# Kernel optimization log

Hardware: AMD Instinct MI355X
Metric: run time of the kernel (lower is better)

The kernel has to match this reference:

```python
import jax, jax.numpy as jnp
import numpy as np

B, T, D, H = 4, 2048, 1024, 16
Dh = D // H          # 64 head dim
NF = Dh // 2         # 32 rotary frequencies


def setup_inputs() -> dict:
    key = jax.random.key(0)
    k0, k1, k2, k3 = jax.random.split(key, 4)
    x = jax.random.normal(k0, (B, T, D), dtype=jnp.float32)
    # 3D spatial coordinates per token, e.g. voxel positions
    coords = jax.random.uniform(k1, (B, T, 3), dtype=jnp.float32, minval=0.0, maxval=64.0)
    w_scale = 1.0 / np.sqrt(D)
    qkv_w = jax.random.normal(k2, (3 * D, D), dtype=jnp.float32) * w_scale
    qkv_b = jnp.zeros((3 * D,), dtype=jnp.float32)
    proj_w = jax.random.normal(k3, (D, D), dtype=jnp.float32) * w_scale
    proj_b = jnp.zeros((D,), dtype=jnp.float32)
    # mixed-axis rope: frequency f uses coordinate axis (f % 3), geometric period spacing within each axis group
    axes = (jnp.arange(NF) % 3).astype(jnp.int32)
    group = (jnp.arange(NF) // 3).astype(jnp.float32)
    n_per_axis = float(NF) / 3.0
    inv_freq = (10000.0 ** (-group / n_per_axis)).astype(jnp.float32)
    return {"x": x, "coords": coords, "qkv_w": qkv_w, "qkv_b": qkv_b,
            "proj_w": proj_w, "proj_b": proj_b, "inv_freq": inv_freq, "axes": axes}


def _apply_rope(t, sin, cos):
    # t: [B, H, T, Dh]; sin/cos: [B, 1, T, Dh//2]  (rotate-half convention)
    t1, t2 = jnp.split(t, 2, axis=-1)
    return jnp.concatenate([t1 * cos - t2 * sin, t1 * sin + t2 * cos], axis=-1)


def reference(x, coords, qkv_w, qkv_b, proj_w, proj_b, inv_freq, axes):
    b, t, d = x.shape
    # fused QKV projection
    qkv = (x @ qkv_w.T + qkv_b).reshape(b, t, 3, H, Dh)
    qkv = jnp.transpose(qkv, (2, 0, 3, 1, 4))     # [3, B, H, T, Dh]
    q, k, v = qkv[0], qkv[1], qkv[2]
    # vectorized per-sample rope from coords (replaces python loop over batch)
    ang = jnp.take(coords, axes, axis=-1) * inv_freq      # [B, T, NF]
    sin = jnp.sin(ang)[:, None]                            # [B, 1, T, NF]
    cos = jnp.cos(ang)[:, None]
    q = _apply_rope(q, sin, cos)
    k = _apply_rope(k, sin, cos)
    # standard scaling mode: single 1/sqrt(Dh) inside SDPA
    scale = 1.0 / np.sqrt(Dh)
    scores = jnp.einsum('bhqd,bhkd->bhqk', q, k) * scale
    attn = jax.nn.softmax(scores, axis=-1)
    out = jnp.einsum('bhqk,bhkd->bhqd', attn, v)           # [B, H, T, Dh]
    out = jnp.transpose(out, (0, 2, 1, 3)).reshape(b, t, d)
    return out @ proj_w.T + proj_b
```

## Files before the change

### kernel.cpp

```cpp
#include <hip/hip_runtime.h>
#include <hip/hip_bf16.h>

#define B_ 4
#define T_ 2048
#define D_ 1024
#define H_ 16
#define DH 64
#define NF 32
#define BH (B_*H_)
#define M_ROWS (B_*T_)

#define QSCALE 0.125f

using u16 = unsigned short;
using u32 = unsigned int;

typedef __bf16 bf16x8 __attribute__((ext_vector_type(8)));
typedef float  f32x4  __attribute__((ext_vector_type(4)));
typedef float  f32x16 __attribute__((ext_vector_type(16)));

__device__ __forceinline__ u16 f2bf(float f) {
  u32 u = __float_as_uint(f);
  u32 r = u + 0x7fffu + ((u >> 16) & 1u);
  return (u16)(r >> 16);
}
__device__ __forceinline__ u16 f2bf_hw(float f) {
  __bf16 h = (__bf16)f;
  return *(u16*)&h;
}
__device__ __forceinline__ u32 pack2(float lo, float hi) {
  return (u32)f2bf_hw(lo) | ((u32)f2bf_hw(hi) << 16);
}
__device__ __forceinline__ float bf2f(u16 h) {
  return __uint_as_float(((u32)h) << 16);
}

__device__ __forceinline__ void pl32swap(u32 a, u32 b, u32& x, u32& y) {
  x = a; y = b;
  asm("s_nop 1\n\t"
      "v_permlane32_swap_b32 %0, %1"
      : "+v"(x), "+v"(y));
}

__device__ __forceinline__ void gload_lds16(const void* g, void* l) {
  __builtin_amdgcn_global_load_lds((__attribute__((address_space(1))) void*)(g),
                                   (__attribute__((address_space(3))) void*)(l),
                                   16, 0, 0);
}

__global__ __launch_bounds__(256)
void cvt_kernel(const float* __restrict__ in, u16* __restrict__ out, int n8) {
  int idx = blockIdx.x * 256 + threadIdx.x;
  if (idx >= n8) return;
  const float4* p = (const float4*)in + (long)idx * 2;
  float4 a = p[0], b = p[1];
  u32 o0 = (u32)f2bf(a.x) | ((u32)f2bf(a.y) << 16);
  u32 o1 = (u32)f2bf(a.z) | ((u32)f2bf(a.w) << 16);
  u32 o2 = (u32)f2bf(b.x) | ((u32)f2bf(b.y) << 16);
  u32 o3 = (u32)f2bf(b.z) | ((u32)f2bf(b.w) << 16);
  ((uint4*)out)[idx] = make_uint4(o0, o1, o2, o3);
}

__global__ __launch_bounds__(256)
void sincos_kernel(const float* __restrict__ coords, const float* __restrict__ inv_freq,
                   const int* __restrict__ axes, float* __restrict__ sc) {
  int idx = blockIdx.x * 256 + threadIdx.x;
  if (idx >= B_ * T_ * NF) return;
  int f = idx & 31;
  long bt = idx >> 5;
  float c = coords[bt * 3 + axes[f]];
  float ang = c * inv_freq[f];
  sc[bt * 64 + f]      = sinf(ang);
  sc[bt * 64 + 32 + f] = cosf(ang);
}

__global__ __launch_bounds__(256, 2)
void gemm_qkv(const u16* __restrict__ A, const u16* __restrict__ Bt,
              const float* __restrict__ bias, const float* __restrict__ sc,
              u16* __restrict__ qr, u16* __restrict__ kr, u16* __restrict__ vbuf) {
  const int N = 3 * D_, K = D_;
  __shared__ u16 As[128 * 64];
  __shared__ u16 Bs[128 * 64];
  int nb = N >> 7;
  int bid = blockIdx.x;
  int nwg = gridDim.x;
  int cpx = nwg >> 3;
  bid = (bid & 7) * cpx + (bid >> 3);
  int bm = bid / nb, bn = bid % nb;
  long m0 = (long)bm << 7, n0 = (long)bn << 7;
  int tid = threadIdx.x;
  int lane = tid & 63, w = tid >> 6;
  int g = lane >> 4, lr = lane & 15;
  int wm = w >> 1, wn = w & 1;

  f32x4 acc[4][4] = {};

  for (int kt = 0; kt < K; kt += 64) {
    __syncthreads();
    #pragma unroll
    for (int j = 0; j < 4; ++j) {
      int ob = j * 4096 + tid * 16;
      int row = ob >> 7, col = (ob & 127) >> 1;
      u16* ldsA = As + j * 2048 + w * 512;
      u16* ldsB = Bs + j * 2048 + w * 512;
      gload_lds16(A + (m0 + row) * K + kt + col, ldsA);
      gload_lds16(Bt + (n0 + row) * K + kt + col, ldsB);
    }
    __syncthreads();
    #pragma unroll
    for (int kk = 0; kk < 2; ++kk) {
      bf16x8 af[4], bfr[4];
      #pragma unroll
      for (int i = 0; i < 4; ++i)
        af[i] = *(const bf16x8*)(As + (wm * 64 + i * 16 + lr) * 64 + kk * 32 + g * 8);
      #pragma unroll
      for (int i = 0; i < 4; ++i)
        bfr[i] = *(const bf16x8*)(Bs + (wn * 64 + i * 16 + lr) * 64 + kk * 32 + g * 8);
      #pragma unroll
      for (int mi = 0; mi < 4; ++mi)
        #pragma unroll
        for (int nj = 0; nj < 4; ++nj)
          acc[mi][nj] = __builtin_amdgcn_mfma_f32_16x16x32_bf16(af[mi], bfr[nj], acc[mi][nj], 0, 0, 0);
    }
  }

  int part = (int)(n0 >> 10);
  int h = ((int)(n0 & 1023) >> 6) + wn;
  float bv[4];
  #pragma unroll
  for (int nj = 0; nj < 4; ++nj)
    bv[nj] = bias[n0 + wn * 64 + nj * 16 + lr];

  #pragma unroll
  for (int mi = 0; mi < 4; ++mi) {
    #pragma unroll
    for (int i = 0; i < 4; ++i) {
      long row = m0 + wm * 64 + mi * 16 + g * 4 + i;
      int b = (int)(row >> 11), t = (int)(row & 2047);
      long obase = ((long)(b * 16 + h) * T_ + t) * 64;
      if (part == 2) {
        #pragma unroll
        for (int nj = 0; nj < 4; ++nj)
          vbuf[obase + nj * 16 + lr] = f2bf(acc[mi][nj][i] + bv[nj]);
      } else {
        u16* outp = part ? kr : qr;
        float fac = part ? 1.0f : QSCALE;
        const float* scp = sc + row * 64;
        #pragma unroll
        for (int nj = 0; nj < 2; ++nj) {
          int d = nj * 16 + lr;
          float sn = scp[d], cs = scp[32 + d];
          float t1 = acc[mi][nj][i]     + bv[nj];
          float t2 = acc[mi][nj + 2][i] + bv[nj + 2];
          outp[obase + d]      = f2bf((t1 * cs - t2 * sn) * fac);
          outp[obase + 32 + d] = f2bf((t1 * sn + t2 * cs) * fac);
        }
      }
    }
  }
}

__global__ __launch_bounds__(256, 2)
void gemm_bt(const u16* __restrict__ A, const u16* __restrict__ Bt,
             const float* __restrict__ bias, float* __restrict__ Cout,
             int M, int N, int K) {
  __shared__ u16 As[128 * 64];
  __shared__ u16 Bs[128 * 64];
  int nb = N >> 7;
  int bid = blockIdx.x;
  int nwg = gridDim.x;
  if ((nwg & 7) == 0) {
    int c = nwg >> 3;
    bid = (bid & 7) * c + (bid >> 3);
  }
  int bm = bid / nb, bn = bid % nb;
  long m0 = (long)bm << 7, n0 = (long)bn << 7;
  int tid = threadIdx.x;
  int lane = tid & 63, w = tid >> 6;
  int g = lane >> 4, lr = lane & 15;
  int wm = w >> 1, wn = w & 1;

  f32x4 acc[4][4] = {};

  for (int kt = 0; kt < K; kt += 64) {
    __syncthreads();
    #pragma unroll
    for (int j = 0; j < 4; ++j) {
      int ob = j * 4096 + tid * 16;
      int row = ob >> 7, col = (ob & 127) >> 1;
      u16* ldsA = As + j * 2048 + w * 512;
      u16* ldsB = Bs + j * 2048 + w * 512;
      gload_lds16(A + (m0 + row) * K + kt + col, ldsA);
      gload_lds16(Bt + (n0 + row) * K + kt + col, ldsB);
    }
    __syncthreads();
    #pragma unroll
    for (int kk = 0; kk < 2; ++kk) {
      bf16x8 af[4], bfr[4];
      #pragma unroll
      for (int i = 0; i < 4; ++i)
        af[i] = *(const bf16x8*)(As + (wm * 64 + i * 16 + lr) * 64 + kk * 32 + g * 8);
      #pragma unroll
      for (int i = 0; i < 4; ++i)
        bfr[i] = *(const bf16x8*)(Bs + (wn * 64 + i * 16 + lr) * 64 + kk * 32 + g * 8);
      #pragma unroll
      for (int mi = 0; mi < 4; ++mi)
        #pragma unroll
        for (int nj = 0; nj < 4; ++nj)
          acc[mi][nj] = __builtin_amdgcn_mfma_f32_16x16x32_bf16(af[mi], bfr[nj], acc[mi][nj], 0, 0, 0);
    }
  }
  #pragma unroll
  for (int mi = 0; mi < 4; ++mi) {
    #pragma unroll
    for (int nj = 0; nj < 4; ++nj) {
      long col = n0 + wn * 64 + nj * 16 + lr;
      float bvv = bias[col];
      #pragma unroll
      for (int i = 0; i < 4; ++i) {
        long row = m0 + wm * 64 + mi * 16 + g * 4 + i;
        Cout[row * (long)N + col] = acc[mi][nj][i] + bvv;
      }
    }
  }
}

__global__ __launch_bounds__(256)
void vtrans_kernel(const u16* __restrict__ vbuf, u16* __restrict__ vt) {
  __shared__ u16 Vsm[128 * 72];
  int bh = blockIdx.y;
  int t0 = blockIdx.x << 7;
  int tid = threadIdx.x;
  #pragma unroll
  for (int it = 0; it < 4; ++it) {
    int item = it * 256 + tid;
    int tl = item >> 3, dg = item & 7;
    uint4 u = *(const uint4*)(vbuf + ((long)bh * T_ + t0 + tl) * 64 + dg * 8);
    *(uint4*)(Vsm + tl * 72 + dg * 8) = u;
  }
  __syncthreads();
  int d = tid >> 2, tc = tid & 3;
  long obase = ((long)bh * DH + d) * T_ + t0 + tc * 32;
  #pragma unroll
  for (int c = 0; c < 4; ++c) {
    u32 o[4];
    #pragma unroll
    for (int j = 0; j < 4; ++j) {
      u16 lo = Vsm[(tc * 32 + c * 8 + 2 * j)     * 72 + d];
      u16 hi = Vsm[(tc * 32 + c * 8 + 2 * j + 1) * 72 + d];
      o[j] = (u32)lo | ((u32)hi << 16);
    }
    *(uint4*)(vt + obase + c * 8) = make_uint4(o[0], o[1], o[2], o[3]);
  }
}

__global__ __launch_bounds__(256, 2)
void attn_kernel(const u16* __restrict__ Qr, const u16* __restrict__ Kr,
                 const u16* __restrict__ Vt, u16* __restrict__ Aout) {
  __shared__ u16 Ks[2][64 * 64];
  __shared__ u16 Vs[2][64 * 64];
  int wg = (blockIdx.x & 7) * 64 + (blockIdx.x >> 3);
  int bh = wg >> 3;
  int b = bh >> 4, h = bh & 15;
  int q0 = (wg & 7) << 8;
  int tid = threadIdx.x;
  int lane = tid & 63, w = tid >> 6;
  int l5 = lane & 31, hb = lane >> 5;

  const long tbase = (long)bh * T_;
  const long vbase = (long)bh * DH;
  const int qs = q0 + w * 64;

  bf16x8 bq0[4], bq1[4];
  #pragma unroll
  for (int s = 0; s < 4; ++s) {
    bq0[s] = *(const bf16x8*)(Qr + (tbase + qs + l5)      * DH + s * 16 + hb * 8);
    bq1[s] = *(const bf16x8*)(Qr + (tbase + qs + 32 + l5) * DH + s * 16 + hb * 8);
  }

  f32x16 oa00 = {}, oa01 = {};
  f32x16 oa10 = {}, oa11 = {};
  float ls0 = 0.f, ls1 = 0.f;

  const int sl = l5 & 7;

  auto STAGE = [&](int buf, int kb) {
    #pragma unroll
    for (int j = 0; j < 2; ++j) {
      int ob = j * 4096 + tid * 16;
      int row = ob >> 7;
      int c = ((ob >> 4) & 7) ^ (row & 7);
      u16* ldsK = Ks[buf] + j * 2048 + w * 512;
      u16* ldsV = Vs[buf] + j * 2048 + w * 512;
      gload_lds16(Kr + (tbase + kb + row) * DH + c * 8, ldsK);
      gload_lds16(Vt + (vbase + row) * T_ + kb + c * 8, ldsV);
    }
  };

  STAGE(0, 0);
  asm volatile("s_waitcnt vmcnt(0)" ::: "memory");
  __builtin_amdgcn_s_barrier();
  __builtin_amdgcn_sched_barrier(0);

  int cur = 0;
  for (int kt = 0; kt < T_ / 64; ++kt) {
    if (kt + 1 < T_ / 64) STAGE(cur ^ 1, (kt + 1) * 64);

    const u16* kbuf = Ks[cur];
    const u16* vbuf = Vs[cur];

    f32x16 p00 = {}, p01 = {}, p10 = {}, p11 = {};
    #pragma unroll
    for (int s = 0; s < 4; ++s) {
      int c = ((2 * s + hb) ^ sl) * 8;
      bf16x8 ak0 = *(const bf16x8*)(kbuf + l5 * 64 + c);
      bf16x8 ak1 = *(const bf16x8*)(kbuf + (32 + l5) * 64 + c);
      p00 = __builtin_amdgcn_mfma_f32_32x32x16_bf16(ak0, bq0[s], p00, 0, 0, 0);
      p01 = __builtin_amdgcn_mfma_f32_32x32x16_bf16(ak1, bq0[s], p01, 0, 0, 0);
      p10 = __builtin_amdgcn_mfma_f32_32x32x16_bf16(ak0, bq1[s], p10, 0, 0, 0);
      p11 = __builtin_amdgcn_mfma_f32_32x32x16_bf16(ak1, bq1[s], p11, 0, 0, 0);
    }

    u32 pA0[8], pB0[8], pA1[8], pB1[8];
    #pragma unroll
    for (int r4 = 0; r4 < 4; ++r4) {
      float a0 = __expf(p00[4 * r4 + 0]), a1 = __expf(p00[4 * r4 + 1]);
      float a2 = __expf(p00[4 * r4 + 2]), a3 = __expf(p00[4 * r4 + 3]);
      ls0 += (a0 + a1) + (a2 + a3);
      pA0[r4] = pack2(a0, a1); pB0[r4] = pack2(a2, a3);
      float b0 = __expf(p01[4 * r4 + 0]), b1 = __expf(p01[4 * r4 + 1]);
      float b2 = __expf(p01[4 * r4 + 2]), b3 = __expf(p01[4 * r4 + 3]);
      ls0 += (b0 + b1) + (b2 + b3);
      pA0[4 + r4] = pack2(b0, b1); pB0[4 + r4] = pack2(b2, b3);
      float c0 = __expf(p10[4 * r4 + 0]), c1 = __expf(p10[4 * r4 + 1]);
      float c2 = __expf(p10[4 * r4 + 2]), c3 = __expf(p10[4 * r4 + 3]);
      ls1 += (c0 + c1) + (c2 + c3);
      pA1[r4] = pack2(c0, c1); pB1[r4] = pack2(c2, c3);
      float d0 = __expf(p11[4 * r4 + 0]), d1 = __expf(p11[4 * r4 + 1]);
      float d2 = __expf(p11[4 * r4 + 2]), d3 = __expf(p11[4 * r4 + 3]);
      ls1 += (d0 + d1) + (d2 + d3);
      pA1[4 + r4] = pack2(d0, d1); pB1[4 + r4] = pack2(d2, d3);
    }

    #pragma unroll
    for (int s2 = 0; s2 < 4; ++s2) {
      int c = ((2 * s2 + hb) ^ sl) * 8;
      bf16x8 av0 = *(const bf16x8*)(vbuf + l5 * 64 + c);
      bf16x8 av1 = *(const bf16x8*)(vbuf + (32 + l5) * 64 + c);
      u32 w0, w1, w2, w3;
      pl32swap(pA0[2 * s2], pA0[2 * s2 + 1], w0, w2);
      pl32swap(pB0[2 * s2], pB0[2 * s2 + 1], w1, w3);
      union { u32 u[4]; bf16x8 v; } bw0;
      bw0.u[0] = w0; bw0.u[1] = w1; bw0.u[2] = w2; bw0.u[3] = w3;
      oa00 = __builtin_amdgcn_mfma_f32_32x32x16_bf16(av0, bw0.v, oa00, 0, 0, 0);
      oa01 = __builtin_amdgcn_mfma_f32_32x32x16_bf16(av1, bw0.v, oa01, 0, 0, 0);
      pl32swap(pA1[2 * s2], pA1[2 * s2 + 1], w0, w2);
      pl32swap(pB1[2 * s2], pB1[2 * s2 + 1], w1, w3);
      union { u32 u[4]; bf16x8 v; } bw1;
      bw1.u[0] = w0; bw1.u[1] = w1; bw1.u[2] = w2; bw1.u[3] = w3;
      oa10 = __builtin_amdgcn_mfma_f32_32x32x16_bf16(av0, bw1.v, oa10, 0, 0, 0);
      oa11 = __builtin_amdgcn_mfma_f32_32x32x16_bf16(av1, bw1.v, oa11, 0, 0, 0);
    }

    __builtin_amdgcn_sched_barrier(0);
    asm volatile("s_waitcnt vmcnt(0)" ::: "memory");
    __builtin_amdgcn_s_barrier();
    __builtin_amdgcn_sched_barrier(0);
    cur ^= 1;
  }

  ls0 += __shfl_xor(ls0, 32);
  ls1 += __shfl_xor(ls1, 32);
  float inv0 = 1.0f / ls0;
  float inv1 = 1.0f / ls1;
  long row0 = (long)b * T_ + qs + l5;
  u16* ob0 = Aout + row0 * D_ + h * DH;
  u16* ob1 = ob0 + 32 * D_;
  #pragma unroll
  for (int r4 = 0; r4 < 4; ++r4) {
    u32 w0 = pack2(oa00[4 * r4 + 0] * inv0, oa00[4 * r4 + 1] * inv0);
    u32 w1 = pack2(oa00[4 * r4 + 2] * inv0, oa00[4 * r4 + 3] * inv0);
    *(uint2*)(ob0 + r4 * 8 + hb * 4) = make_uint2(w0, w1);
    u32 w2 = pack2(oa01[4 * r4 + 0] * inv0, oa01[4 * r4 + 1] * inv0);
    u32 w3 = pack2(oa01[4 * r4 + 2] * inv0, oa01[4 * r4 + 3] * inv0);
    *(uint2*)(ob0 + 32 + r4 * 8 + hb * 4) = make_uint2(w2, w3);
    u32 w4 = pack2(oa10[4 * r4 + 0] * inv1, oa10[4 * r4 + 1] * inv1);
    u32 w5 = pack2(oa10[4 * r4 + 2] * inv1, oa10[4 * r4 + 3] * inv1);
    *(uint2*)(ob1 + r4 * 8 + hb * 4) = make_uint2(w4, w5);
    u32 w6 = pack2(oa11[4 * r4 + 0] * inv1, oa11[4 * r4 + 1] * inv1);
    u32 w7 = pack2(oa11[4 * r4 + 2] * inv1, oa11[4 * r4 + 3] * inv1);
    *(uint2*)(ob1 + 32 + r4 * 8 + hb * 4) = make_uint2(w6, w7);
  }
}

extern "C" void kernel_launch(void* const* d_in, const int* in_sizes, int n_in,
                              void* d_out, int out_size, void* d_ws, size_t ws_size,
                              hipStream_t stream) {
  const float* x        = (const float*)d_in[0];
  const float* coords   = (const float*)d_in[1];
  const float* qkv_w    = (const float*)d_in[2];
  const float* qkv_b    = (const float*)d_in[3];
  const float* proj_w   = (const float*)d_in[4];
  const float* proj_b   = (const float*)d_in[5];
  const float* inv_freq = (const float*)d_in[6];
  const int*   axes     = (const int*)d_in[7];
  float* out = (float*)d_out;

  char* ws = (char*)d_ws;
  size_t off = 0;
  auto alloc = [&](size_t bytes) -> char* {
    char* p = ws + off;
    off += (bytes + 255) & ~(size_t)255;
    return p;
  };
  u16*   xb     = (u16*)  alloc((size_t)M_ROWS * D_ * 2);
  u16*   wqkv   = (u16*)  alloc((size_t)3 * D_ * D_ * 2);
  u16*   wproj  = (u16*)  alloc((size_t)D_ * D_ * 2);
  float* sc     = (float*)alloc((size_t)M_ROWS * 64 * 4);
  u16*   qr     = (u16*)  alloc((size_t)BH * T_ * DH * 2);
  u16*   kr     = (u16*)  alloc((size_t)BH * T_ * DH * 2);
  u16*   vbuf   = (u16*)  alloc((size_t)BH * T_ * DH * 2);
  u16*   vt     = (u16*)  alloc((size_t)BH * T_ * DH * 2);
  u16*   aout   = vbuf;

  cvt_kernel<<<(M_ROWS * D_ / 8 + 255) / 256, 256, 0, stream>>>(x, xb, M_ROWS * D_ / 8);
  cvt_kernel<<<(3 * D_ * D_ / 8 + 255) / 256, 256, 0, stream>>>(qkv_w, wqkv, 3 * D_ * D_ / 8);
  cvt_kernel<<<(D_ * D_ / 8 + 255) / 256, 256, 0, stream>>>(proj_w, wproj, D_ * D_ / 8);
  sincos_kernel<<<(B_ * T_ * NF + 255) / 256, 256, 0, stream>>>(coords, inv_freq, axes, sc);

  gemm_qkv<<<(M_ROWS / 128) * (3 * D_ / 128), 256, 0, stream>>>(xb, wqkv, qkv_b, sc,
                                                                qr, kr, vbuf);
  vtrans_kernel<<<dim3(T_ / 128, BH), 256, 0, stream>>>(vbuf, vt);
  attn_kernel<<<512, 256, 0, stream>>>(qr, kr, vt, aout);
  gemm_bt<<<(M_ROWS / 128) * (D_ / 128), 256, 0, stream>>>(aout, wproj, proj_b, out,
                                                           M_ROWS, D_, D_);
}
```

Baseline: 214.4 us.

## Fuse V transpose into QKV GEMM epilogue and stage 128-key blocks in attention

The QKV GEMM epilogue now stages each V head tile in the reused shared memory and writes it out already transposed. This removes the separate vtrans kernel and the round trip of V through an intermediate buffer. Separately, the attention kernel loads K/V in 128-key chunks (two 64-key sub-tiles per stage), halving the number of barrier/wait iterations at the cost of doubling LDS use per workgroup. The larger LDS footprint (64 KB) may limit occupancy, and the GEMM epilogue gains extra syncs for V tiles.

```diff
diff --git a/kernel.cpp b/kernel.cpp
--- a/kernel.cpp
+++ b/kernel.cpp
@@ -77,10 +77,11 @@
 __global__ __launch_bounds__(256, 2)
 void gemm_qkv(const u16* __restrict__ A, const u16* __restrict__ Bt,
               const float* __restrict__ bias, const float* __restrict__ sc,
-              u16* __restrict__ qr, u16* __restrict__ kr, u16* __restrict__ vbuf) {
+              u16* __restrict__ qr, u16* __restrict__ kr, u16* __restrict__ vt) {
   const int N = 3 * D_, K = D_;
-  __shared__ u16 As[128 * 64];
-  __shared__ u16 Bs[128 * 64];
+  __shared__ u16 SMEM[128 * 64 * 2];
+  u16* As = SMEM;
+  u16* Bs = SMEM + 128 * 64;
   int nb = N >> 7;
   int bid = blockIdx.x;
   int nwg = gridDim.x;
@@ -125,26 +126,54 @@
   }
 
   int part = (int)(n0 >> 10);
-  int h = ((int)(n0 & 1023) >> 6) + wn;
+  int b = (int)(m0 >> 11), t0 = (int)(m0 & 2047);
   float bv[4];
   #pragma unroll
   for (int nj = 0; nj < 4; ++nj)
     bv[nj] = bias[n0 + wn * 64 + nj * 16 + lr];
 
-  #pragma unroll
-  for (int mi = 0; mi < 4; ++mi) {
-    #pragma unroll
-    for (int i = 0; i < 4; ++i) {
-      long row = m0 + wm * 64 + mi * 16 + g * 4 + i;
-      int b = (int)(row >> 11), t = (int)(row & 2047);
-      long obase = ((long)(b * 16 + h) * T_ + t) * 64;
-      if (part == 2) {
+  if (part == 2) {
+    int h0 = (int)((n0 & 1023) >> 6);
+    u16* Vsm = SMEM;
+    #pragma unroll
+    for (int hsel = 0; hsel < 2; ++hsel) {
+      __syncthreads();
+      if (wn == hsel) {
         #pragma unroll
-        for (int nj = 0; nj < 4; ++nj)
-          vbuf[obase + nj * 16 + lr] = f2bf(acc[mi][nj][i] + bv[nj]);
-      } else {
-        u16* outp = part ? kr : qr;
-        float fac = part ? 1.0f : QSCALE;
+        for (int mi = 0; mi < 4; ++mi)
+          #pragma unroll
+          for (int i = 0; i < 4; ++i) {
+            int lrow = wm * 64 + mi * 16 + g * 4 + i;
+            #pragma unroll
+            for (int nj = 0; nj < 4; ++nj)
+              Vsm[lrow * 72 + nj * 16 + lr] = f2bf(acc[mi][nj][i] + bv[nj]);
+          }
+      }
+      __syncthreads();
+      int d = tid >> 2, tc = tid & 3;
+      long obase = ((long)((b * 16 + h0 + hsel) * DH + d)) * T_ + t0 + tc * 32;
+      #pragma unroll
+      for (int c = 0; c < 4; ++c) {
+        u32 o[4];
+        #pragma unroll
+        for (int j = 0; j < 4; ++j) {
+          u16 lo = Vsm[(tc * 32 + c * 8 + 2 * j)     * 72 + d];
+          u16 hi = Vsm[(tc * 32 + c * 8 + 2 * j + 1) * 72 + d];
+          o[j] = (u32)lo | ((u32)hi << 16);
+        }
+        *(uint4*)(vt + obase + c * 8) = make_uint4(o[0], o[1], o[2], o[3]);
+      }
+    }
+  } else {
+    int h = ((int)(n0 & 1023) >> 6) + wn;
+    u16* outp = part ? kr : qr;
+    float fac = part ? 1.0f : QSCALE;
+    #pragma unroll
+    for (int mi = 0; mi < 4; ++mi) {
+      #pragma unroll
+      for (int i = 0; i < 4; ++i) {
+        long row = m0 + wm * 64 + mi * 16 + g * 4 + i;
+        long obase = ((long)((b * 16 + h)) * T_ + (row & 2047)) * 64;
         const float* scp = sc + row * 64;
         #pragma unroll
         for (int nj = 0; nj < 2; ++nj) {
@@ -225,40 +254,11 @@
   }
 }
 
-__global__ __launch_bounds__(256)
-void vtrans_kernel(const u16* __restrict__ vbuf, u16* __restrict__ vt) {
-  __shared__ u16 Vsm[128 * 72];
-  int bh = blockIdx.y;
-  int t0 = blockIdx.x << 7;
-  int tid = threadIdx.x;
-  #pragma unroll
-  for (int it = 0; it < 4; ++it) {
-    int item = it * 256 + tid;
-    int tl = item >> 3, dg = item & 7;
-    uint4 u = *(const uint4*)(vbuf + ((long)bh * T_ + t0 + tl) * 64 + dg * 8);
-    *(uint4*)(Vsm + tl * 72 + dg * 8) = u;
-  }
-  __syncthreads();
-  int d = tid >> 2, tc = tid & 3;
-  long obase = ((long)bh * DH + d) * T_ + t0 + tc * 32;
-  #pragma unroll
-  for (int c = 0; c < 4; ++c) {
-    u32 o[4];
-    #pragma unroll
-    for (int j = 0; j < 4; ++j) {
-      u16 lo = Vsm[(tc * 32 + c * 8 + 2 * j)     * 72 + d];
-      u16 hi = Vsm[(tc * 32 + c * 8 + 2 * j + 1) * 72 + d];
-      o[j] = (u32)lo | ((u32)hi << 16);
-    }
-    *(uint4*)(vt + obase + c * 8) = make_uint4(o[0], o[1], o[2], o[3]);
-  }
-}
-
 __global__ __launch_bounds__(256, 2)
 void attn_kernel(const u16* __restrict__ Qr, const u16* __restrict__ Kr,
                  const u16* __restrict__ Vt, u16* __restrict__ Aout) {
-  __shared__ u16 Ks[2][64 * 64];
-  __shared__ u16 Vs[2][64 * 64];
+  __shared__ u16 Ks[2][2][64 * 64];
+  __shared__ u16 Vs[2][2][64 * 64];
   int wg = (blockIdx.x & 7) * 64 + (blockIdx.x >> 3);
   int bh = wg >> 3;
   int b = bh >> 4, h = bh & 15;
@@ -286,14 +286,17 @@
 
   auto STAGE = [&](int buf, int kb) {
     #pragma unroll
-    for (int j = 0; j < 2; ++j) {
-      int ob = j * 4096 + tid * 16;
-      int row = ob >> 7;
-      int c = ((ob >> 4) & 7) ^ (row & 7);
-      u16* ldsK = Ks[buf] + j * 2048 + w * 512;
-      u16* ldsV = Vs[buf] + j * 2048 + w * 512;
-      gload_lds16(Kr + (tbase + kb + row) * DH + c * 8, ldsK);
-      gload_lds16(Vt + (vbase + row) * T_ + kb + c * 8, ldsV);
+    for (int sub = 0; sub < 2; ++sub) {
+      #pragma unroll
+      for (int j = 0; j < 2; ++j) {
+        int ob = j * 4096 + tid * 16;
+        int row = ob >> 7;
+        int c = ((ob >> 4) & 7) ^ (row & 7);
+        u16* ldsK = Ks[buf][sub] + j * 2048 + w * 512;
+        u16* ldsV = Vs[buf][sub] + j * 2048 + w * 512;
+        gload_lds16(Kr + (tbase + kb + sub * 64 + row) * DH + c * 8, ldsK);
+        gload_lds16(Vt + (vbase + row) * T_ + kb + sub * 64 + c * 8, ldsV);
+      }
     }
   };
 
@@ -303,63 +306,66 @@
   __builtin_amdgcn_sched_barrier(0);
 
   int cur = 0;
-  for (int kt = 0; kt < T_ / 64; ++kt) {
-    if (kt + 1 < T_ / 64) STAGE(cur ^ 1, (kt + 1) * 64);
-
-    const u16* kbuf = Ks[cur];
-    const u16* vbuf = Vs[cur];
-
-    f32x16 p00 = {}, p01 = {}, p10 = {}, p11 = {};
-    #pragma unroll
-    for (int s = 0; s < 4; ++s) {
-      int c = ((2 * s + hb) ^ sl) * 8;
-      bf16x8 ak0 = *(const bf16x8*)(kbuf + l5 * 64 + c);
-      bf16x8 ak1 = *(const bf16x8*)(kbuf + (32 + l5) * 64 + c);
-      p00 = __builtin_amdgcn_mfma_f32_32x32x16_bf16(ak0, bq0[s], p00, 0, 0, 0);
-      p01 = __builtin_amdgcn_mfma_f32_32x32x16_bf16(ak1, bq0[s], p01, 0, 0, 0);
-      p10 = __builtin_amdgcn_mfma_f32_32x32x16_bf16(ak0, bq1[s], p10, 0, 0, 0);
-      p11 = __builtin_amdgcn_mfma_f32_32x32x16_bf16(ak1, bq1[s], p11, 0, 0, 0);
-    }
-
-    u32 pA0[8], pB0[8], pA1[8], pB1[8];
-    #pragma unroll
-    for (int r4 = 0; r4 < 4; ++r4) {
-      float a0 = __expf(p00[4 * r4 + 0]), a1 = __expf(p00[4 * r4 + 1]);
-      float a2 = __expf(p00[4 * r4 + 2]), a3 = __expf(p00[4 * r4 + 3]);
-      ls0 += (a0 + a1) + (a2 + a3);
-      pA0[r4] = pack2(a0, a1); pB0[r4] = pack2(a2, a3);
-      float b0 = __expf(p01[4 * r4 + 0]), b1 = __expf(p01[4 * r4 + 1]);
-      float b2 = __expf(p01[4 * r4 + 2]), b3 = __expf(p01[4 * r4 + 3]);
-      ls0 += (b0 + b1) + (b2 + b3);
-      pA0[4 + r4] = pack2(b0, b1); pB0[4 + r4] = pack2(b2, b3);
-      float c0 = __expf(p10[4 * r4 + 0]), c1 = __expf(p10[4 * r4 + 1]);
-      float c2 = __expf(p10[4 * r4 + 2]), c3 = __expf(p10[4 * r4 + 3]);
-      ls1 += (c0 + c1) + (c2 + c3);
-      pA1[r4] = pack2(c0, c1); pB1[r4] = pack2(c2, c3);
-      float d0 = __expf(p11[4 * r4 + 0]), d1 = __expf(p11[4 * r4 + 1]);
-      float d2 = __expf(p11[4 * r4 + 2]), d3 = __expf(p11[4 * r4 + 3]);
-      ls1 += (d0 + d1) + (d2 + d3);
-      pA1[4 + r4] = pack2(d0, d1); pB1[4 + r4] = pack2(d2, d3);
-    }
-
-    #pragma unroll
-    for (int s2 = 0; s2 < 4; ++s2) {
-      int c = ((2 * s2 + hb) ^ sl) * 8;
-      bf16x8 av0 = *(const bf16x8*)(vbuf + l5 * 64 + c);
-      bf16x8 av1 = *(const bf16x8*)(vbuf + (32 + l5) * 64 + c);
-      u32 w0, w1, w2, w3;
-      pl32swap(pA0[2 * s2], pA0[2 * s2 + 1], w0, w2);
-      pl32swap(pB0[2 * s2], pB0[2 * s2 + 1], w1, w3);
-      union { u32 u[4]; bf16x8 v; } bw0;
-      bw0.u[0] = w0; bw0.u[1] = w1; bw0.u[2] = w2; bw0.u[3] = w3;
-      oa00 = __builtin_amdgcn_mfma_f32_32x32x16_bf16(av0, bw0.v, oa00, 0, 0, 0);
-      oa01 = __builtin_amdgcn_mfma_f32_32x32x16_bf16(av1, bw0.v, oa01, 0, 0, 0);
-      pl32swap(pA1[2 * s2], pA1[2 * s2 + 1], w0, w2);
-      pl32swap(pB1[2 * s2], pB1[2 * s2 + 1], w1, w3);
-      union { u32 u[4]; bf16x8 v; } bw1;
-      bw1.u[0] = w0; bw1.u[1] = w1; bw1.u[2] = w2; bw1.u[3] = w3;
-      oa10 = __builtin_amdgcn_mfma_f32_32x32x16_bf16(av0, bw1.v, oa10, 0, 0, 0);
-      oa11 = __builtin_amdgcn_mfma_f32_32x32x16_bf16(av1, bw1.v, oa11, 0, 0, 0);
+  for (int kt = 0; kt < T_ / 128; ++kt) {
+    if (kt + 1 < T_ / 128) STAGE(cur ^ 1, (kt + 1) * 128);
+
+    #pragma unroll
+    for (int h2 = 0; h2 < 2; ++h2) {
+      const u16* kbuf = Ks[cur][h2];
+      const u16* vbuf = Vs[cur][h2];
+
+      f32x16 p00 = {}, p01 = {}, p10 = {}, p11 = {};
+      #pragma unroll
+      for (int s = 0; s < 4; ++s) {
+        int c = ((2 * s + hb) ^ sl) * 8;
+        bf16x8 ak0 = *(const bf16x8*)(kbuf + l5 * 64 + c);
+        bf16x8 ak1 = *(const bf16x8*)(kbuf + (32 + l5) * 64 + c);
+        p00 = __builtin_amdgcn_mfma_f32_32x32x16_bf16(ak0, bq0[s], p00, 0, 0, 0);
+        p01 = __builtin_amdgcn_mfma_f32_32x32x16_bf16(ak1, bq0[s], p01, 0, 0, 0);
+        p10 = __builtin_amdgcn_mfma_f32_32x32x16_bf16(ak0, bq1[s], p10, 0, 0, 0);
+        p11 = __builtin_amdgcn_mfma_f32_32x32x16_bf16(ak1, bq1[s], p11, 0, 0, 0);
+      }
+
+      u32 pA0[8], pB0[8], pA1[8], pB1[8];
+      #pragma unroll
+      for (int r4 = 0; r4 < 4; ++r4) {
+        float a0 = __expf(p00[4 * r4 + 0]), a1 = __expf(p00[4 * r4 + 1]);
+        float a2 = __expf(p00[4 * r4 + 2]), a3 = __expf(p00[4 * r4 + 3]);
+        ls0 += (a0 + a1) + (a2 + a3);
+        pA0[r4] = pack2(a0, a1); pB0[r4] = pack2(a2, a3);
+        float b0 = __expf(p01[4 * r4 + 0]), b1 = __expf(p01[4 * r4 + 1]);
+        float b2 = __expf(p01[4 * r4 + 2]), b3 = __expf(p01[4 * r4 + 3]);
+        ls0 += (b0 + b1) + (b2 + b3);
+        pA0[4 + r4] = pack2(b0, b1); pB0[4 + r4] = pack2(b2, b3);
+        float c0 = __expf(p10[4 * r4 + 0]), c1 = __expf(p10[4 * r4 + 1]);
+        float c2 = __expf(p10[4 * r4 + 2]), c3 = __expf(p10[4 * r4 + 3]);
+        ls1 += (c0 + c1) + (c2 + c3);
+        pA1[r4] = pack2(c0, c1); pB1[r4] = pack2(c2, c3);
+        float d0 = __expf(p11[4 * r4 + 0]), d1 = __expf(p11[4 * r4 + 1]);
+        float d2 = __expf(p11[4 * r4 + 2]), d3 = __expf(p11[4 * r4 + 3]);
+        ls1 += (d0 + d1) + (d2 + d3);
+        pA1[4 + r4] = pack2(d0, d1); pB1[4 + r4] = pack2(d2, d3);
+      }
+
+      #pragma unroll
+      for (int s2 = 0; s2 < 4; ++s2) {
+        int c = ((2 * s2 + hb) ^ sl) * 8;
+        bf16x8 av0 = *(const bf16x8*)(vbuf + l5 * 64 + c);
+        bf16x8 av1 = *(const bf16x8*)(vbuf + (32 + l5) * 64 + c);
+        u32 w0, w1, w2, w3;
+        pl32swap(pA0[2 * s2], pA0[2 * s2 + 1], w0, w2);
+        pl32swap(pB0[2 * s2], pB0[2 * s2 + 1], w1, w3);
+        union { u32 u[4]; bf16x8 v; } bw0;
+        bw0.u[0] = w0; bw0.u[1] = w1; bw0.u[2] = w2; bw0.u[3] = w3;
+        oa00 = __builtin_amdgcn_mfma_f32_32x32x16_bf16(av0, bw0.v, oa00, 0, 0, 0);
+        oa01 = __builtin_amdgcn_mfma_f32_32x32x16_bf16(av1, bw0.v, oa01, 0, 0, 0);
+        pl32swap(pA1[2 * s2], pA1[2 * s2 + 1], w0, w2);
+        pl32swap(pB1[2 * s2], pB1[2 * s2 + 1], w1, w3);
+        union { u32 u[4]; bf16x8 v; } bw1;
+        bw1.u[0] = w0; bw1.u[1] = w1; bw1.u[2] = w2; bw1.u[3] = w3;
+        oa10 = __builtin_amdgcn_mfma_f32_32x32x16_bf16(av0, bw1.v, oa10, 0, 0, 0);
+        oa11 = __builtin_amdgcn_mfma_f32_32x32x16_bf16(av1, bw1.v, oa11, 0, 0, 0);
+      }
     }
 
     __builtin_amdgcn_sched_barrier(0);
@@ -419,9 +425,8 @@
   float* sc     = (float*)alloc((size_t)M_ROWS * 64 * 4);
   u16*   qr     = (u16*)  alloc((size_t)BH * T_ * DH * 2);
   u16*   kr     = (u16*)  alloc((size_t)BH * T_ * DH * 2);
-  u16*   vbuf   = (u16*)  alloc((size_t)BH * T_ * DH * 2);
   u16*   vt     = (u16*)  alloc((size_t)BH * T_ * DH * 2);
-  u16*   aout   = vbuf;
+  u16*   aout   = (u16*)  alloc((size_t)BH * T_ * DH * 2);
 
   cvt_kernel<<<(M_ROWS * D_ / 8 + 255) / 256, 256, 0, stream>>>(x, xb, M_ROWS * D_ / 8);
   cvt_kernel<<<(3 * D_ * D_ / 8 + 255) / 256, 256, 0, stream>>>(qkv_w, wqkv, 3 * D_ * D_ / 8);
@@ -429,8 +434,7 @@
   sincos_kernel<<<(B_ * T_ * NF + 255) / 256, 256, 0, stream>>>(coords, inv_freq, axes, sc);
 
   gemm_qkv<<<(M_ROWS / 128) * (3 * D_ / 128), 256, 0, stream>>>(xb, wqkv, qkv_b, sc,
-                                                                qr, kr, vbuf);
-  vtrans_kernel<<<dim3(T_ / 128, BH), 256, 0, stream>>>(vbuf, vt);
+                                                                qr, kr, vt);
   attn_kernel<<<512, 256, 0, stream>>>(qr, kr, vt, aout);
   gemm_bt<<<(M_ROWS / 128) * (D_ / 128), 256, 0, stream>>>(aout, wproj, proj_b, out,
                                                            M_ROWS, D_, D_);
```

Result: faster. 203.8 us (-4.9%).
